# Performance work log

Measured on AMD Instinct MI355X. Metric: run time of the kernel, lower is better.

## Reference

```python
import jax, jax.numpy as jnp
import numpy as np

H, C, L = 2, 32, 25
EPS = 1e-5


def setup_inputs() -> dict:
    key = jax.random.key(0)
    ks = jax.random.split(key, 12)
    N, E = 20000, 100000
    x_input = jax.random.normal(ks[0], (N, 5), jnp.float32)
    # edges with no self loops (module uses add_self_loops=True, which first removes them)
    src = jax.random.randint(ks[1], (L, E), 0, N, dtype=jnp.int32)
    off = jax.random.randint(ks[2], (L, E), 1, N, dtype=jnp.int32)
    dst = (src + off) % N
    edge_indices = jnp.stack([src, dst], axis=1)              # [L, 2, E]
    edge_weights = jax.random.uniform(ks[3], (L, E, 1), jnp.float32)
    g = lambda k, shp, fan: jax.random.normal(k, shp, jnp.float32) / np.float32(np.sqrt(fan))
    return {
        "x_input": x_input,
        "edge_indices": edge_indices,
        "edge_weights": edge_weights,
        "Wl": g(ks[4], (L, 5, H * C), 5),
        "bl": jnp.zeros((L, H * C), jnp.float32),
        "Wr": g(ks[5], (L, 5, H * C), 5),
        "br": jnp.zeros((L, H * C), jnp.float32),
        "We": g(ks[6], (L, 1, H * C), 1),
        "att": g(ks[7], (L, H, C), C),
        "conv_bias": jnp.zeros((L, C), jnp.float32),
        "gamma1": jnp.ones((L, C), jnp.float32),
        "beta1": jnp.zeros((L, C), jnp.float32),
        "W1": g(ks[8], (800, 800), 800),
        "b1": jnp.zeros((800,), jnp.float32),
        "W2": g(ks[9], (800, 5), 800),
        "b2": jnp.zeros((5,), jnp.float32),
    }


def reference(x_input, edge_indices, edge_weights, Wl, bl, Wr, br, We, att,
              conv_bias, gamma1, beta1, W1, b1, W2, b2):
    N = x_input.shape[0]
    loops = jnp.arange(N, dtype=edge_indices.dtype)

    def layer(carry, p):
        ei, ew, wl, bl_, wr, br_, we, a, cb, g_, be_ = p
        src, dst = ei[0], ei[1]
        ones_e = jnp.ones((src.shape[0],), x_input.dtype)
        # add_self_loops with fill_value='mean': loop attr = mean of incoming edge attrs
        cnt = jax.ops.segment_sum(ones_e, dst, num_segments=N)
        loop_attr = jax.ops.segment_sum(ew, dst, num_segments=N) / jnp.maximum(cnt, 1.0)[:, None]
        s2 = jnp.concatenate([src, loops])
        d2 = jnp.concatenate([dst, loops])
        ea = jnp.concatenate([ew, loop_attr], axis=0)          # [E+N, 1]
        xl = (x_input @ wl + bl_).reshape(N, H, C)             # source transform
        xr = (x_input @ wr + br_).reshape(N, H, C)             # target transform
        eh = jax.nn.leaky_relu(xl[s2] + xr[d2] + (ea @ we).reshape(-1, H, C), 0.2)
        alpha = jnp.einsum('ehc,hc->eh', eh, a)                # [E+N, H]
        amax = jax.ops.segment_max(alpha, d2, num_segments=N)
        alpha = jnp.exp(alpha - amax[d2])
        alpha = alpha / jax.ops.segment_sum(alpha, d2, num_segments=N)[d2]
        msg = (xl[s2] * alpha[:, :, None]).reshape(-1, H * C)
        deg = jax.ops.segment_sum(jnp.ones((s2.shape[0],), x_input.dtype), d2, num_segments=N)
        out = (jax.ops.segment_sum(msg, d2, num_segments=N) / deg[:, None]).reshape(N, H, C)
        out = out.mean(axis=1) + cb                            # concat=False -> mean over heads, + bias
        mu = out.mean(axis=0)
        var = out.var(axis=0)                                  # BatchNorm1d, training-mode batch stats
        out = g_ * (out - mu) * jax.lax.rsqrt(var + EPS) + be_
        return carry, jax.nn.leaky_relu(out, 0.01)

    _, hs = jax.lax.scan(layer, None,
                         (edge_indices, edge_weights, Wl, bl, Wr, br, We, att,
                          conv_bias, gamma1, beta1))            # [L, N, C]
    h = jnp.transpose(hs, (1, 0, 2)).reshape(N, L * C)          # cat along feature dim
    h = jax.nn.relu(h @ W1 + b1)
    return h @ W2 + b2
```

## Files before the change

### kernel.cpp

```cpp
#include <hip/hip_runtime.h>
#include <hip/hip_bf16.h>

#define N_NODES 20000
#define N_EDGES 100000
#define N_LAYERS 25
#define NPAD 20096
#define EPS_BN 1e-5f
#define LOG2E 1.44269504088896340736f
#define NL_NN (N_LAYERS * N_NODES)
#define TOTAL_E (N_LAYERS * N_EDGES)
#define TOTAL_SLOTS (TOTAL_E + NL_NN)
#define SCAN_BLKS ((NL_NN + 1023) / 1024)
#define QUARTER_N 5000
#define CNT_BLKS (N_LAYERS * 4)
#define W1T_END (CNT_BLKS + 700)
#define XPAD_END (W1T_END + 157)
#define HPAD_BLKS 75
#define PREP_BLKS (XPAD_END + HPAD_BLKS)
#define EDGE_BLKS ((TOTAL_E + 1023) / 1024)
#define FILL_BLKS (EDGE_BLKS + SCAN_BLKS)
#define NGRP 14
#define NPW 8
#define NPL (N_NODES / NPW)
#define ATTN_WAVES (NL_NN / NPW)
#define ATTN_BLKS (ATTN_WAVES / 4)
#define G1_BLKS (7 * 157)

typedef short short8 __attribute__((ext_vector_type(8)));
typedef short short4v __attribute__((ext_vector_type(4)));
typedef float floatx4 __attribute__((ext_vector_type(4)));
typedef float float8v __attribute__((ext_vector_type(8)));
typedef int int8v __attribute__((ext_vector_type(8)));
typedef int int2v __attribute__((ext_vector_type(2)));

template <int PAT>
__device__ __forceinline__ float swz(float v) {
  return __int_as_float(__builtin_amdgcn_ds_swizzle(__float_as_int(v), PAT));
}

template <int CTRL>
__device__ __forceinline__ float dpp_add(float v) {
  int r = __builtin_amdgcn_update_dpp(0, __float_as_int(v), CTRL, 0xF, 0xF, true);
  return v + __int_as_float(r);
}

__device__ __forceinline__ float xadd16(float p) {
#if __has_builtin(__builtin_amdgcn_permlane16_swap)
  int2v r = __builtin_amdgcn_permlane16_swap(__float_as_int(p),
                                             __float_as_int(p), false, false);
  return __int_as_float(r[0]) + __int_as_float(r[1]);
#else
  return p + swz<0x401F>(p);
#endif
}

__device__ __forceinline__ float ldbf(const unsigned short* __restrict__ p, int idx) {
  return __uint_as_float((unsigned)p[idx] << 16);
}

__device__ __forceinline__ unsigned short bfbits(float v) {
  return __builtin_bit_cast(unsigned short, (__hip_bfloat16)v);
}

__device__ __forceinline__ void gl_lds16(const short* g, short* l) {
  __builtin_amdgcn_global_load_lds(
      (const __attribute__((address_space(1))) void*)g,
      (__attribute__((address_space(3))) void*)l, 16, 0, 0);
}

__device__ __forceinline__ int8v sload8(const void* p) {
  int8v r;
  asm volatile(
      "s_load_dwordx8 %0, %1, 0x0\n\t"
      "s_waitcnt lgkmcnt(0)"
      : "=s"(r)
      : "s"(p));
  return r;
}

__device__ __forceinline__ void sload_rp(const void* p, int8v& a, int8v& b) {
  asm volatile(
      "s_load_dwordx8 %0, %2, 0x0\n\t"
      "s_load_dwordx8 %1, %2, 0x20\n\t"
      "s_waitcnt lgkmcnt(0)"
      : "=s"(a), "=s"(b)
      : "s"(p));
}

__device__ __forceinline__ void sload_chunk(const void* p, int8v& r0, int8v& r1,
                                            int8v& r2, int8v& r3) {
  asm volatile(
      "s_load_dwordx8 %0, %4, 0x0\n\t"
      "s_load_dwordx8 %1, %4, 0x20\n\t"
      "s_load_dwordx8 %2, %4, 0x40\n\t"
      "s_load_dwordx8 %3, %4, 0x60\n\t"
      "s_waitcnt lgkmcnt(0)"
      : "=s"(r0), "=s"(r1), "=s"(r2), "=s"(r3)
      : "s"(p));
}

__device__ __forceinline__ void red4(float& p0, float& p1, float& p2, float& p3) {
  asm volatile(
      "s_nop 1\n\t"
      "v_add_f32_dpp %0, %0, %0 quad_perm:[1,0,3,2] row_mask:0xf bank_mask:0xf\n\t"
      "v_add_f32_dpp %1, %1, %1 quad_perm:[1,0,3,2] row_mask:0xf bank_mask:0xf\n\t"
      "v_add_f32_dpp %2, %2, %2 quad_perm:[1,0,3,2] row_mask:0xf bank_mask:0xf\n\t"
      "v_add_f32_dpp %3, %3, %3 quad_perm:[1,0,3,2] row_mask:0xf bank_mask:0xf\n\t"
      "v_add_f32_dpp %0, %0, %0 quad_perm:[2,3,0,1] row_mask:0xf bank_mask:0xf\n\t"
      "v_add_f32_dpp %1, %1, %1 quad_perm:[2,3,0,1] row_mask:0xf bank_mask:0xf\n\t"
      "v_add_f32_dpp %2, %2, %2 quad_perm:[2,3,0,1] row_mask:0xf bank_mask:0xf\n\t"
      "v_add_f32_dpp %3, %3, %3 quad_perm:[2,3,0,1] row_mask:0xf bank_mask:0xf\n\t"
      "v_add_f32_dpp %0, %0, %0 row_half_mirror row_mask:0xf bank_mask:0xf\n\t"
      "v_add_f32_dpp %1, %1, %1 row_half_mirror row_mask:0xf bank_mask:0xf\n\t"
      "v_add_f32_dpp %2, %2, %2 row_half_mirror row_mask:0xf bank_mask:0xf\n\t"
      "v_add_f32_dpp %3, %3, %3 row_half_mirror row_mask:0xf bank_mask:0xf\n\t"
      "v_add_f32_dpp %0, %0, %0 row_mirror row_mask:0xf bank_mask:0xf\n\t"
      "v_add_f32_dpp %1, %1, %1 row_mirror row_mask:0xf bank_mask:0xf\n\t"
      "v_add_f32_dpp %2, %2, %2 row_mirror row_mask:0xf bank_mask:0xf\n\t"
      "v_add_f32_dpp %3, %3, %3 row_mirror row_mask:0xf bank_mask:0xf\n\t"
      "s_nop 1"
      : "+v"(p0), "+v"(p1), "+v"(p2), "+v"(p3));
}

__global__ __launch_bounds__(1024) void prep_kernel(
    const int* __restrict__ ei, const float* __restrict__ ew,
    const float* __restrict__ x, const float* __restrict__ W1,
    int* __restrict__ cnt, int* __restrict__ rank,
    float* __restrict__ wsumg, float* __restrict__ xpad,
    __hip_bfloat16* __restrict__ W1bT, unsigned short* __restrict__ hn) {
  __shared__ int smem[QUARTER_N];
  __shared__ float fsm[QUARTER_N];
  int b = blockIdx.x;
  if (b < CNT_BLKS) {
    int l = b >> 2, base = (b & 3) * QUARTER_N;
    for (int i = threadIdx.x; i < QUARTER_N; i += 1024) {
      smem[i] = 0;
      fsm[i] = 0.f;
    }
    __syncthreads();
    const int* dstp = ei + (size_t)l * 2 * N_EDGES + N_EDGES;
    const float* ewp = ew + (size_t)l * N_EDGES;
    int* rkp = rank + l * N_EDGES;
    for (int e = threadIdx.x; e < N_EDGES; e += 1024) {
      int d = dstp[e] - base;
      if ((unsigned)d < (unsigned)QUARTER_N) {
        rkp[e] = atomicAdd(&smem[d], 1);
        atomicAdd(&fsm[d], ewp[e]);
      }
    }
    __syncthreads();
    int* outp = cnt + l * N_NODES + base;
    float* wp = wsumg + l * N_NODES + base;
    for (int i = threadIdx.x; i < QUARTER_N; i += 1024) {
      outp[i] = smem[i];
      wp[i] = fsm[i];
    }
  } else if (b < W1T_END) {
    float* tile = (float*)smem;
    int bb = b - CNT_BLKS;
    int j0 = (bb % 28) * 32, k0 = (bb / 28) * 32;
    int tx = threadIdx.x & 31, ty = threadIdx.x >> 5;
    tile[ty * 33 + tx] = (j0 + tx < 800) ? W1[(k0 + ty) * 800 + j0 + tx] : 0.f;
    __syncthreads();
    W1bT[(size_t)(j0 + ty) * 800 + k0 + tx] = (__hip_bfloat16)tile[tx * 33 + ty];
  } else if (b < XPAD_END) {
    int idx = (b - W1T_END) * 1024 + threadIdx.x;
    if (idx < N_NODES * 8) {
      int nn = idx >> 3, k = idx & 7;
      xpad[idx] = (k < 5) ? x[nn * 5 + k] : 0.f;
    }
  } else {
    int idx = (b - XPAD_END) * 1024 + threadIdx.x;
    const int per_l = (NPAD - N_NODES) * 32;
    if (idx < N_LAYERS * per_l) {
      int l = idx / per_l;
      int rem = idx - l * per_l;
      hn[((size_t)l * NPAD + N_NODES) * 32 + rem] = 0;
    }
  }
}

__global__ __launch_bounds__(1024) void scan_a(const int* __restrict__ cnt,
                                               int* __restrict__ scn,
                                               int* __restrict__ btot,
                                               float* __restrict__ gsum,
                                               float* __restrict__ gsumsq) {
  int t = threadIdx.x, b = blockIdx.x;
  int i = b * 1024 + t;
  int lane = t & 63, wv = t >> 6;
  int v = (i < NL_NN) ? cnt[i] + 1 : 0;
  int sc = v;
#pragma unroll
  for (int off = 1; off < 64; off <<= 1) {
    int u = __shfl_up(sc, off);
    if (lane >= off) sc += u;
  }
  __shared__ int ws[16];
  if (lane == 63) ws[wv] = sc;
  __syncthreads();
  if (t < 16) {
    int xx = ws[t];
#pragma unroll
    for (int off = 1; off < 16; off <<= 1) {
      int u = __shfl_up(xx, off);
      if (t >= off) xx += u;
    }
    ws[t] = xx;
  }
  __syncthreads();
  int bofs = wv ? ws[wv - 1] : 0;
  if (i < NL_NN) scn[i] = bofs + sc - v;
  if (t == 0) btot[b] = ws[15];
  if (b == 200 && t < N_LAYERS * 32) {
    gsum[t] = 0.f;
    gsumsq[t] = 0.f;
  }
}

__global__ __launch_bounds__(512) void scan_b(const int* __restrict__ btot,
                                              int* __restrict__ boff) {
  int t = threadIdx.x;
  int lane = t & 63, wv = t >> 6;
  int v = (t < SCAN_BLKS) ? btot[t] : 0;
  int sc = v;
#pragma unroll
  for (int off = 1; off < 64; off <<= 1) {
    int u = __shfl_up(sc, off);
    if (lane >= off) sc += u;
  }
  __shared__ int ws[8];
  if (lane == 63) ws[wv] = sc;
  __syncthreads();
  if (t < 8) {
    int xx = ws[t];
#pragma unroll
    for (int off = 1; off < 8; off <<= 1) {
      int u = __shfl_up(xx, off);
      if (t >= off) xx += u;
    }
    ws[t] = xx;
  }
  __syncthreads();
  int bofs = wv ? ws[wv - 1] : 0;
  if (t < SCAN_BLKS) boff[t] = bofs + sc - v;
}

__global__ __launch_bounds__(1024) void fill_kernel(const int* __restrict__ ei,
                                                    const float* __restrict__ ew,
                                                    const int* __restrict__ scn,
                                                    const int* __restrict__ boff,
                                                    const int* __restrict__ rank,
                                                    const float* __restrict__ wsumg,
                                                    const float* __restrict__ xpad,
                                                    int* __restrict__ rowptr,
                                                    float* __restrict__ epf) {
  int b = blockIdx.x;
  if (b < EDGE_BLKS) {
    int idx = b * 1024 + threadIdx.x;
    if (idx >= TOTAL_E) return;
    int l = idx / N_EDGES, e = idx - l * N_EDGES;
    int src = ei[(size_t)l * 2 * N_EDGES + e];
    int dst = ei[(size_t)l * 2 * N_EDGES + N_EDGES + e];
    int g = l * N_NODES + dst;
    int pos = scn[g] + boff[g >> 10] + rank[idx];
    float w = ew[(size_t)l * N_EDGES + e];
    float4 xv = *(const float4*)(xpad + (size_t)src * 8);
    float x4v = xpad[(size_t)src * 8 + 4];
    float8v r;
    r[0] = w; r[1] = xv.x; r[2] = xv.y; r[3] = xv.z; r[4] = xv.w; r[5] = x4v;
    r[6] = 0.f; r[7] = 0.f;
    *(float8v*)(epf + (size_t)pos * 8) = r;
  } else {
    int i = (b - EDGE_BLKS) * 1024 + threadIdx.x;
    if (i < NL_NN) {
      int st = scn[i] + boff[i >> 10];
      int en = (i + 1 < NL_NN) ? scn[i + 1] + boff[(i + 1) >> 10] : TOTAL_SLOTS;
      rowptr[i] = st;
      int cw = en - st - 1;
      float wm = wsumg[i] * __builtin_amdgcn_rcpf(fmaxf((float)cw, 1.f));
      int n = i - (i / N_NODES) * N_NODES;
      float4 xv = *(const float4*)(xpad + (size_t)n * 8);
      float x4v = xpad[(size_t)n * 8 + 4];
      float8v r;
      r[0] = wm; r[1] = xv.x; r[2] = xv.y; r[3] = xv.z; r[4] = xv.w; r[5] = x4v;
      r[6] = 0.f; r[7] = 0.f;
      *(float8v*)(epf + (size_t)(en - 1) * 8) = r;
    }
    if (i < 31) rowptr[NL_NN + i] = TOTAL_SLOTS;
    if (i < 4) {
      float8v z = {0.f, 0.f, 0.f, 0.f, 0.f, 0.f, 0.f, 0.f};
      *(float8v*)(epf + (size_t)(TOTAL_SLOTS + i) * 8) = z;
    }
  }
}

__global__ __launch_bounds__(256) void attn_kernel(
    const float* __restrict__ xpad, const int* __restrict__ rowptr,
    const float* __restrict__ epf,
    const float* __restrict__ Wl, const float* __restrict__ bl,
    const float* __restrict__ Wr, const float* __restrict__ br,
    const float* __restrict__ We, const float* __restrict__ att,
    const float* __restrict__ cbias, unsigned short* __restrict__ out_pre,
    float* __restrict__ gsum, float* __restrict__ gsumsq) {
  int b = blockIdx.x;
  const int q = ATTN_BLKS >> 3, r = ATTN_BLKS & 7;
  int xcd = b & 7, ib = b >> 3;
  int nb = (xcd < r ? xcd * (q + 1) : r * (q + 1) + (xcd - r) * q) + ib;
  int wid = __builtin_amdgcn_readfirstlane(nb * 4 + (threadIdx.x >> 6));
  int lane = threadIdx.x & 63;
  int l = wid / NPL;
  int n0 = (wid - l * NPL) * NPW;

  float wlv0 = Wl[(l * 5 + 0) * 64 + lane];
  float wlv1 = Wl[(l * 5 + 1) * 64 + lane];
  float wlv2 = Wl[(l * 5 + 2) * 64 + lane];
  float wlv3 = Wl[(l * 5 + 3) * 64 + lane];
  float wlv4 = Wl[(l * 5 + 4) * 64 + lane];
  float wr0 = Wr[(l * 5 + 0) * 64 + lane];
  float wr1 = Wr[(l * 5 + 1) * 64 + lane];
  float wr2 = Wr[(l * 5 + 2) * 64 + lane];
  float wr3 = Wr[(l * 5 + 3) * 64 + lane];
  float wr4 = Wr[(l * 5 + 4) * 64 + lane];
  float blv = bl[l * 64 + lane];
  float brv = br[l * 64 + lane];
  float wev = We[l * 64 + lane];
  float att2v = att[l * 64 + lane] * LOG2E;
  float cbv = cbias[l * 32 + (lane & 31)];

  int8v rpa, rpb;
  sload_rp(rowptr + (size_t)wid * 8, rpa, rpb);

  float s1 = 0.f, s2 = 0.f;

#pragma unroll
  for (int i = 0; i < NPW; i++) {
    int st = rpa[i & 7];
    int en = (i == 7) ? rpb[0] : rpa[(i + 1) & 7];
    int valid = en - st;

    int8v xn = sload8(xpad + (size_t)(n0 + i) * 8);
    float xrn = brv;
    xrn = fmaf(__int_as_float(xn[0]), wr0, xrn);
    xrn = fmaf(__int_as_float(xn[1]), wr1, xrn);
    xrn = fmaf(__int_as_float(xn[2]), wr2, xrn);
    xrn = fmaf(__int_as_float(xn[3]), wr3, xrn);
    xrn = fmaf(__int_as_float(xn[4]), wr4, xrn);

    float ssum = 0.f, acc = 0.f;
    int nchunk = (valid + 3) >> 2;
    for (int c = 0; c < nchunk; c++) {
      int8v r0, r1, r2, r3;
      sload_chunk(epf + (size_t)(st + c * 4) * 8, r0, r1, r2, r3);
      int m = valid - c * 4;
      float xa[4], pk[4];
#pragma unroll
      for (int k = 0; k < 4; k++) {
        int8v rr = (k == 0) ? r0 : (k == 1) ? r1 : (k == 2) ? r2 : r3;
        float a = fmaf(__int_as_float(rr[1]), wlv0, blv);
        a = fmaf(__int_as_float(rr[2]), wlv1, a);
        a = fmaf(__int_as_float(rr[3]), wlv2, a);
        a = fmaf(__int_as_float(rr[4]), wlv3, a);
        a = fmaf(__int_as_float(rr[5]), wlv4, a);
        xa[k] = a;
        float v = a + fmaf(__int_as_float(rr[0]), wev, xrn);
        float lk = fmaxf(v, 0.2f * v);
        pk[k] = lk * att2v;
      }
      red4(pk[0], pk[1], pk[2], pk[3]);
#pragma unroll
      for (int k = 0; k < 4; k++) pk[k] = xadd16(pk[k]);
#pragma unroll
      for (int k = 0; k < 4; k++) {
        float pe = __builtin_amdgcn_exp2f(pk[k]);
        pe = (k < m) ? pe : 0.f;
        ssum += pe;
        acc = fmaf(xa[k], pe, acc);
      }
    }
    float outv = acc * __builtin_amdgcn_rcpf(ssum * (float)valid);
    float o2 = outv + __shfl_xor(outv, 32);
    float oval = 0.5f * o2 + cbv;
    if (lane < 32)
      out_pre[((size_t)wid * NPW + i) * 32 + lane] = bfbits(oval);
    s1 += oval;
    s2 = fmaf(oval, oval, s2);
  }
  if (lane < 32) {
    atomicAdd(&gsum[l * 32 + lane], s1);
    atomicAdd(&gsumsq[l * 32 + lane], s2);
  }
}

__global__ __launch_bounds__(256) void norm_kernel(const unsigned short* __restrict__ out_pre,
                                                   const float* __restrict__ gsum,
                                                   const float* __restrict__ gsumsq,
                                                   const float* __restrict__ gamma,
                                                   const float* __restrict__ beta,
                                                   unsigned short* __restrict__ hn) {
  int idx = blockIdx.x * 256 + threadIdx.x;
  int l = idx / (N_NODES * 8);
  int rem = idx - l * (N_NODES * 8);
  int n = rem >> 3, q = rem & 7;
  int c0 = q * 4;
  short4v v4 = *(const short4v*)(out_pre + (l * N_NODES + n) * 32 + c0);
  short4v o;
#pragma unroll
  for (int i = 0; i < 4; i++) {
    int c = c0 + i;
    float mu = gsum[l * 32 + c] * (1.f / N_NODES);
    float var = gsumsq[l * 32 + c] * (1.f / N_NODES) - mu * mu;
    float vv = __uint_as_float((unsigned)(unsigned short)v4[i] << 16);
    float v = gamma[l * 32 + c] * (vv - mu) * rsqrtf(var + EPS_BN) + beta[l * 32 + c];
    v = v > 0.f ? v : 0.01f * v;
    o[i] = (short)bfbits(v);
  }
  *(short4v*)(hn + ((size_t)l * NPAD + n) * 32 + c0) = o;
}

__global__ __launch_bounds__(256) void gemm1_kernel(const short* __restrict__ hn,
                                                    const short* __restrict__ W1bT,
                                                    const float* __restrict__ b1,
                                                    const float* __restrict__ W2,
                                                    float* __restrict__ p) {
  __shared__ __align__(16) short As[128 * 32];
  __shared__ __align__(16) short Bs[128 * 32];
  const int q = G1_BLKS >> 3, r = G1_BLKS & 7;
  int bf = blockIdx.x;
  int xcd = bf & 7, ib = bf >> 3;
  int nb = (xcd < r ? xcd * (q + 1) : r * (q + 1) + (xcd - r) * q) + ib;
  int mt = nb / 7, nt = nb - mt * 7;
  int n0 = nt * 128, m0 = mt * 128;
  int t = threadIdx.x;
  int wave = t >> 6, lane = t & 63;
  int wr = wave >> 1, wc = wave & 1;
  int mrow = lane & 15, quad = lane >> 4;
  floatx4 acc[4][4];
#pragma unroll
  for (int i = 0; i < 4; i++)
#pragma unroll
    for (int j = 0; j < 4; j++) acc[i][j] = (floatx4){0.f, 0.f, 0.f, 0.f};

  int r0 = t >> 2, s0 = t & 3;
  int r1 = (t + 256) >> 2, s1 = (t + 256) & 3;
  const short* aG0 = hn + (m0 + r0) * 32 + s0 * 8;
  const short* aG1 = hn + (m0 + r1) * 32 + s1 * 8;
  const short* bG0 = W1bT + (n0 + r0) * 800 + s0 * 8;
  const short* bG1 = W1bT + (n0 + r1) * 800 + s1 * 8;
  const int ak = NPAD * 32;
  short* aD0 = As + wave * 512;
  short* aD1 = As + 2048 + wave * 512;
  short* bD0 = Bs + wave * 512;
  short* bD1 = Bs + 2048 + wave * 512;

  for (int kt = 0; kt < 25; kt++) {
    gl_lds16(aG0, aD0);
    gl_lds16(aG1, aD1);
    gl_lds16(bG0, bD0);
    gl_lds16(bG1, bD1);
    aG0 += ak; aG1 += ak; bG0 += 32; bG1 += 32;
    __syncthreads();
    short8 af[4], bfr[4];
#pragma unroll
    for (int i = 0; i < 4; i++)
      af[i] = *(const short8*)(&As[(wr * 64 + i * 16 + mrow) * 32 + quad * 8]);
#pragma unroll
    for (int j = 0; j < 4; j++)
      bfr[j] = *(const short8*)(&Bs[(wc * 64 + j * 16 + mrow) * 32 + quad * 8]);
#pragma unroll
    for (int i = 0; i < 4; i++)
#pragma unroll
      for (int j = 0; j < 4; j++)
        acc[i][j] = __builtin_amdgcn_mfma_f32_16x16x32_bf16(af[i], bfr[j], acc[i][j], 0, 0, 0);
    __syncthreads();
  }

  float w2v[4][5];
  float b1v[4];
#pragma unroll
  for (int j = 0; j < 4; j++) {
    int col = n0 + wc * 64 + j * 16 + mrow;
    bool ok = col < 800;
    b1v[j] = ok ? b1[col] : 0.f;
#pragma unroll
    for (int jj = 0; jj < 5; jj++) w2v[j][jj] = ok ? W2[col * 5 + jj] : 0.f;
  }
  int grp = nt * 2 + wc;
#pragma unroll
  for (int i = 0; i < 4; i++) {
#pragma unroll
    for (int rr = 0; rr < 4; rr++) {
      float s[5] = {0.f, 0.f, 0.f, 0.f, 0.f};
#pragma unroll
      for (int j = 0; j < 4; j++) {
        float v = fmaxf(acc[i][j][rr] + b1v[j], 0.f);
#pragma unroll
        for (int jj = 0; jj < 5; jj++) s[jj] = fmaf(v, w2v[j][jj], s[jj]);
      }
#pragma unroll
      for (int jj = 0; jj < 5; jj++) {
        s[jj] = dpp_add<0xB1>(s[jj]);
        s[jj] = dpp_add<0x4E>(s[jj]);
        s[jj] = dpp_add<0x141>(s[jj]);
        s[jj] = dpp_add<0x140>(s[jj]);
      }
      int row = m0 + wr * 64 + i * 16 + quad * 4 + rr;
      if (mrow == 0) {
#pragma unroll
        for (int jj = 0; jj < 5; jj++)
          p[(row * NGRP + grp) * 5 + jj] = s[jj];
      }
    }
  }
}

__global__ __launch_bounds__(256) void gemm2r_kernel(const float* __restrict__ p,
                                                     const float* __restrict__ b2,
                                                     float* __restrict__ out) {
  int idx = blockIdx.x * 256 + threadIdx.x;
  if (idx >= N_NODES * 5) return;
  int row = idx / 5, jj = idx - row * 5;
  float s = b2[jj];
#pragma unroll
  for (int g = 0; g < NGRP; g++) s += p[(row * NGRP + g) * 5 + jj];
  out[idx] = s;
}

extern "C" void kernel_launch(void* const* d_in, const int* in_sizes, int n_in,
                              void* d_out, int out_size, void* d_ws, size_t ws_size,
                              hipStream_t stream) {
  const float* x    = (const float*)d_in[0];
  const int*   ei   = (const int*)d_in[1];
  const float* ew   = (const float*)d_in[2];
  const float* Wl   = (const float*)d_in[3];
  const float* bl   = (const float*)d_in[4];
  const float* Wr   = (const float*)d_in[5];
  const float* br   = (const float*)d_in[6];
  const float* We   = (const float*)d_in[7];
  const float* att  = (const float*)d_in[8];
  const float* cb   = (const float*)d_in[9];
  const float* gam  = (const float*)d_in[10];
  const float* bet  = (const float*)d_in[11];
  const float* W1   = (const float*)d_in[12];
  const float* b1   = (const float*)d_in[13];
  const float* W2   = (const float*)d_in[14];
  const float* b2   = (const float*)d_in[15];

  char* ws = (char*)d_ws;
  size_t off = 0;
  auto alloc = [&](size_t bytes) {
    void* p = ws + off;
    off = (off + bytes + 255) & ~(size_t)255;
    return p;
  };
  int* cnt     = (int*)alloc((size_t)NL_NN * 4);
  int* scn     = (int*)alloc((size_t)NL_NN * 4);
  int* btot    = (int*)alloc(SCAN_BLKS * 4);
  int* boff    = (int*)alloc(SCAN_BLKS * 4);
  int* rank    = (int*)alloc((size_t)TOTAL_E * 4);
  int* rowptr  = (int*)alloc((size_t)(NL_NN + 32) * 4);
  float* wsumg = (float*)alloc((size_t)NL_NN * 4);
  float* epf   = (float*)alloc((size_t)TOTAL_SLOTS * 32 + 256);
  unsigned short* out_pre = (unsigned short*)alloc((size_t)NL_NN * 32 * 2);
  float* gsum   = (float*)alloc(N_LAYERS * 32 * 4);
  float* gsumsq = (float*)alloc(N_LAYERS * 32 * 4);
  float* xpad   = (float*)alloc((size_t)N_NODES * 8 * 4);
  __hip_bfloat16* w1t = (__hip_bfloat16*)alloc((size_t)896 * 800 * 2);
  float* pbuf = (float*)alloc((size_t)NPAD * NGRP * 5 * 4);
  unsigned short* hn = (unsigned short*)alloc((size_t)N_LAYERS * NPAD * 32 * 2);

  prep_kernel<<<PREP_BLKS, 1024, 0, stream>>>(ei, ew, x, W1, cnt, rank, wsumg,
                                              xpad, w1t, hn);
  scan_a<<<SCAN_BLKS, 1024, 0, stream>>>(cnt, scn, btot, gsum, gsumsq);
  scan_b<<<1, 512, 0, stream>>>(btot, boff);
  fill_kernel<<<FILL_BLKS, 1024, 0, stream>>>(ei, ew, scn, boff, rank, wsumg,
                                              xpad, rowptr, epf);
  attn_kernel<<<ATTN_BLKS, 256, 0, stream>>>(
      xpad, rowptr, epf, Wl, bl, Wr, br, We, att, cb, out_pre, gsum, gsumsq);
  norm_kernel<<<(NL_NN * 8) / 256, 256, 0, stream>>>(
      out_pre, gsum, gsumsq, gam, bet, hn);
  gemm1_kernel<<<G1_BLKS, 256, 0, stream>>>(
      (const short*)hn, (const short*)w1t, b1, W2, pbuf);
  gemm2r_kernel<<<(N_NODES * 5 + 255) / 256, 256, 0, stream>>>(
      pbuf, b2, (float*)d_out);
}
```

Baseline: 484.3 us.

## Pack per-edge records to 16 bytes with bf16 features, widen attn chunks to 8

The per-edge record written by fill_kernel shrinks from 32 bytes of fp32 to 16 bytes: the edge weight stays fp32 and the five source features are stored as bf16 pairs. attn_kernel now reads 8 edges per scalar-load chunk instead of 4 and reduces 8 logits at once with a wider DPP reduction. BatchNorm partial sums are combined across the block's four waves in shared memory before the atomics, cutting atomic traffic fourfold. The intent is to halve the edge-record bandwidth and amortise reduction and sync work, at the cost of bf16 rounding of the input features and more wasted lanes on short rows.

```diff
diff --git a/kernel.cpp b/kernel.cpp
--- a/kernel.cpp
+++ b/kernel.cpp
@@ -29,9 +29,9 @@
 typedef short short8 __attribute__((ext_vector_type(8)));
 typedef short short4v __attribute__((ext_vector_type(4)));
 typedef float floatx4 __attribute__((ext_vector_type(4)));
-typedef float float8v __attribute__((ext_vector_type(8)));
 typedef int int8v __attribute__((ext_vector_type(8)));
 typedef int int2v __attribute__((ext_vector_type(2)));
+typedef int int4v __attribute__((ext_vector_type(4)));
 
 template <int PAT>
 __device__ __forceinline__ float swz(float v) {
@@ -99,27 +99,45 @@
       : "s"(p));
 }
 
-__device__ __forceinline__ void red4(float& p0, float& p1, float& p2, float& p3) {
+__device__ __forceinline__ void red8(float& p0, float& p1, float& p2, float& p3,
+                                     float& p4, float& p5, float& p6, float& p7) {
   asm volatile(
       "s_nop 1\n\t"
       "v_add_f32_dpp %0, %0, %0 quad_perm:[1,0,3,2] row_mask:0xf bank_mask:0xf\n\t"
       "v_add_f32_dpp %1, %1, %1 quad_perm:[1,0,3,2] row_mask:0xf bank_mask:0xf\n\t"
       "v_add_f32_dpp %2, %2, %2 quad_perm:[1,0,3,2] row_mask:0xf bank_mask:0xf\n\t"
       "v_add_f32_dpp %3, %3, %3 quad_perm:[1,0,3,2] row_mask:0xf bank_mask:0xf\n\t"
+      "v_add_f32_dpp %4, %4, %4 quad_perm:[1,0,3,2] row_mask:0xf bank_mask:0xf\n\t"
+      "v_add_f32_dpp %5, %5, %5 quad_perm:[1,0,3,2] row_mask:0xf bank_mask:0xf\n\t"
+      "v_add_f32_dpp %6, %6, %6 quad_perm:[1,0,3,2] row_mask:0xf bank_mask:0xf\n\t"
+      "v_add_f32_dpp %7, %7, %7 quad_perm:[1,0,3,2] row_mask:0xf bank_mask:0xf\n\t"
       "v_add_f32_dpp %0, %0, %0 quad_perm:[2,3,0,1] row_mask:0xf bank_mask:0xf\n\t"
       "v_add_f32_dpp %1, %1, %1 quad_perm:[2,3,0,1] row_mask:0xf bank_mask:0xf\n\t"
       "v_add_f32_dpp %2, %2, %2 quad_perm:[2,3,0,1] row_mask:0xf bank_mask:0xf\n\t"
       "v_add_f32_dpp %3, %3, %3 quad_perm:[2,3,0,1] row_mask:0xf bank_mask:0xf\n\t"
+      "v_add_f32_dpp %4, %4, %4 quad_perm:[2,3,0,1] row_mask:0xf bank_mask:0xf\n\t"
+      "v_add_f32_dpp %5, %5, %5 quad_perm:[2,3,0,1] row_mask:0xf bank_mask:0xf\n\t"
+      "v_add_f32_dpp %6, %6, %6 quad_perm:[2,3,0,1] row_mask:0xf bank_mask:0xf\n\t"
+      "v_add_f32_dpp %7, %7, %7 quad_perm:[2,3,0,1] row_mask:0xf bank_mask:0xf\n\t"
       "v_add_f32_dpp %0, %0, %0 row_half_mirror row_mask:0xf bank_mask:0xf\n\t"
       "v_add_f32_dpp %1, %1, %1 row_half_mirror row_mask:0xf bank_mask:0xf\n\t"
       "v_add_f32_dpp %2, %2, %2 row_half_mirror row_mask:0xf bank_mask:0xf\n\t"
       "v_add_f32_dpp %3, %3, %3 row_half_mirror row_mask:0xf bank_mask:0xf\n\t"
+      "v_add_f32_dpp %4, %4, %4 row_half_mirror row_mask:0xf bank_mask:0xf\n\t"
+      "v_add_f32_dpp %5, %5, %5 row_half_mirror row_mask:0xf bank_mask:0xf\n\t"
+      "v_add_f32_dpp %6, %6, %6 row_half_mirror row_mask:0xf bank_mask:0xf\n\t"
+      "v_add_f32_dpp %7, %7, %7 row_half_mirror row_mask:0xf bank_mask:0xf\n\t"
       "v_add_f32_dpp %0, %0, %0 row_mirror row_mask:0xf bank_mask:0xf\n\t"
       "v_add_f32_dpp %1, %1, %1 row_mirror row_mask:0xf bank_mask:0xf\n\t"
       "v_add_f32_dpp %2, %2, %2 row_mirror row_mask:0xf bank_mask:0xf\n\t"
       "v_add_f32_dpp %3, %3, %3 row_mirror row_mask:0xf bank_mask:0xf\n\t"
+      "v_add_f32_dpp %4, %4, %4 row_mirror row_mask:0xf bank_mask:0xf\n\t"
+      "v_add_f32_dpp %5, %5, %5 row_mirror row_mask:0xf bank_mask:0xf\n\t"
+      "v_add_f32_dpp %6, %6, %6 row_mirror row_mask:0xf bank_mask:0xf\n\t"
+      "v_add_f32_dpp %7, %7, %7 row_mirror row_mask:0xf bank_mask:0xf\n\t"
       "s_nop 1"
-      : "+v"(p0), "+v"(p1), "+v"(p2), "+v"(p3));
+      : "+v"(p0), "+v"(p1), "+v"(p2), "+v"(p3),
+        "+v"(p4), "+v"(p5), "+v"(p6), "+v"(p7));
 }
 
 __global__ __launch_bounds__(1024) void prep_kernel(
@@ -253,7 +271,7 @@
                                                     const float* __restrict__ wsumg,
                                                     const float* __restrict__ xpad,
                                                     int* __restrict__ rowptr,
-                                                    float* __restrict__ epf) {
+                                                    int* __restrict__ epr) {
   int b = blockIdx.x;
   if (b < EDGE_BLKS) {
     int idx = b * 1024 + threadIdx.x;
@@ -266,10 +284,12 @@
     float w = ew[(size_t)l * N_EDGES + e];
     float4 xv = *(const float4*)(xpad + (size_t)src * 8);
     float x4v = xpad[(size_t)src * 8 + 4];
-    float8v r;
-    r[0] = w; r[1] = xv.x; r[2] = xv.y; r[3] = xv.z; r[4] = xv.w; r[5] = x4v;
-    r[6] = 0.f; r[7] = 0.f;
-    *(float8v*)(epf + (size_t)pos * 8) = r;
+    int4v r;
+    r[0] = __float_as_int(w);
+    r[1] = (int)bfbits(xv.x) | ((int)bfbits(xv.y) << 16);
+    r[2] = (int)bfbits(xv.z) | ((int)bfbits(xv.w) << 16);
+    r[3] = (int)bfbits(x4v);
+    *(int4v*)(epr + (size_t)pos * 4) = r;
   } else {
     int i = (b - EDGE_BLKS) * 1024 + threadIdx.x;
     if (i < NL_NN) {
@@ -281,33 +301,38 @@
       int n = i - (i / N_NODES) * N_NODES;
       float4 xv = *(const float4*)(xpad + (size_t)n * 8);
       float x4v = xpad[(size_t)n * 8 + 4];
-      float8v r;
-      r[0] = wm; r[1] = xv.x; r[2] = xv.y; r[3] = xv.z; r[4] = xv.w; r[5] = x4v;
-      r[6] = 0.f; r[7] = 0.f;
-      *(float8v*)(epf + (size_t)(en - 1) * 8) = r;
+      int4v r;
+      r[0] = __float_as_int(wm);
+      r[1] = (int)bfbits(xv.x) | ((int)bfbits(xv.y) << 16);
+      r[2] = (int)bfbits(xv.z) | ((int)bfbits(xv.w) << 16);
+      r[3] = (int)bfbits(x4v);
+      *(int4v*)(epr + (size_t)(en - 1) * 4) = r;
     }
     if (i < 31) rowptr[NL_NN + i] = TOTAL_SLOTS;
-    if (i < 4) {
-      float8v z = {0.f, 0.f, 0.f, 0.f, 0.f, 0.f, 0.f, 0.f};
-      *(float8v*)(epf + (size_t)(TOTAL_SLOTS + i) * 8) = z;
+    if (i < 8) {
+      int4v z = {0, 0, 0, 0};
+      *(int4v*)(epr + (size_t)(TOTAL_SLOTS + i) * 4) = z;
     }
   }
 }
 
 __global__ __launch_bounds__(256) void attn_kernel(
     const float* __restrict__ xpad, const int* __restrict__ rowptr,
-    const float* __restrict__ epf,
+    const int* __restrict__ epr,
     const float* __restrict__ Wl, const float* __restrict__ bl,
     const float* __restrict__ Wr, const float* __restrict__ br,
     const float* __restrict__ We, const float* __restrict__ att,
     const float* __restrict__ cbias, unsigned short* __restrict__ out_pre,
     float* __restrict__ gsum, float* __restrict__ gsumsq) {
+  __shared__ float sb[256];
   int b = blockIdx.x;
   const int q = ATTN_BLKS >> 3, r = ATTN_BLKS & 7;
   int xcd = b & 7, ib = b >> 3;
   int nb = (xcd < r ? xcd * (q + 1) : r * (q + 1) + (xcd - r) * q) + ib;
-  int wid = __builtin_amdgcn_readfirstlane(nb * 4 + (threadIdx.x >> 6));
-  int lane = threadIdx.x & 63;
+  int tid = threadIdx.x;
+  int w = tid >> 6;
+  int wid = __builtin_amdgcn_readfirstlane(nb * 4 + w);
+  int lane = tid & 63;
   int l = wid / NPL;
   int n0 = (wid - l * NPL) * NPW;
 
@@ -347,30 +372,40 @@
     xrn = fmaf(__int_as_float(xn[4]), wr4, xrn);
 
     float ssum = 0.f, acc = 0.f;
-    int nchunk = (valid + 3) >> 2;
+    int nchunk = (valid + 7) >> 3;
     for (int c = 0; c < nchunk; c++) {
       int8v r0, r1, r2, r3;
-      sload_chunk(epf + (size_t)(st + c * 4) * 8, r0, r1, r2, r3);
-      int m = valid - c * 4;
-      float xa[4], pk[4];
-#pragma unroll
-      for (int k = 0; k < 4; k++) {
-        int8v rr = (k == 0) ? r0 : (k == 1) ? r1 : (k == 2) ? r2 : r3;
-        float a = fmaf(__int_as_float(rr[1]), wlv0, blv);
-        a = fmaf(__int_as_float(rr[2]), wlv1, a);
-        a = fmaf(__int_as_float(rr[3]), wlv2, a);
-        a = fmaf(__int_as_float(rr[4]), wlv3, a);
-        a = fmaf(__int_as_float(rr[5]), wlv4, a);
+      sload_chunk((const char*)epr + (size_t)(st + c * 8) * 16, r0, r1, r2, r3);
+      int m = valid - c * 8;
+      float xa[8], pk[8];
+#define RVEC(k) ((k) < 2 ? r0 : (k) < 4 ? r1 : (k) < 6 ? r2 : r3)
+#define RD(k, j) (RVEC(k)[((k)&1) * 4 + (j)])
+#pragma unroll
+      for (int k = 0; k < 8; k++) {
+        float wgt = __int_as_float(RD(k, 0));
+        int d1 = RD(k, 1), d2 = RD(k, 2), d3 = RD(k, 3);
+        float x0 = __int_as_float(d1 << 16);
+        float x1 = __int_as_float(d1 & (int)0xffff0000);
+        float x2 = __int_as_float(d2 << 16);
+        float x3 = __int_as_float(d2 & (int)0xffff0000);
+        float x4 = __int_as_float(d3 << 16);
+        float a = fmaf(x0, wlv0, blv);
+        a = fmaf(x1, wlv1, a);
+        a = fmaf(x2, wlv2, a);
+        a = fmaf(x3, wlv3, a);
+        a = fmaf(x4, wlv4, a);
         xa[k] = a;
-        float v = a + fmaf(__int_as_float(rr[0]), wev, xrn);
+        float v = a + fmaf(wgt, wev, xrn);
         float lk = fmaxf(v, 0.2f * v);
         pk[k] = lk * att2v;
       }
-      red4(pk[0], pk[1], pk[2], pk[3]);
-#pragma unroll
-      for (int k = 0; k < 4; k++) pk[k] = xadd16(pk[k]);
-#pragma unroll
-      for (int k = 0; k < 4; k++) {
+#undef RVEC
+#undef RD
+      red8(pk[0], pk[1], pk[2], pk[3], pk[4], pk[5], pk[6], pk[7]);
+#pragma unroll
+      for (int k = 0; k < 8; k++) pk[k] = xadd16(pk[k]);
+#pragma unroll
+      for (int k = 0; k < 8; k++) {
         float pe = __builtin_amdgcn_exp2f(pk[k]);
         pe = (k < m) ? pe : 0.f;
         ssum += pe;
@@ -385,9 +420,14 @@
     s1 += oval;
     s2 = fmaf(oval, oval, s2);
   }
-  if (lane < 32) {
-    atomicAdd(&gsum[l * 32 + lane], s1);
-    atomicAdd(&gsumsq[l * 32 + lane], s2);
+  sb[tid] = (lane < 32) ? s1 : s2;
+  __syncthreads();
+  if (tid < 64) {
+    float t = sb[tid] + sb[tid + 64] + sb[tid + 128] + sb[tid + 192];
+    if (tid < 32)
+      atomicAdd(&gsum[l * 32 + tid], t);
+    else
+      atomicAdd(&gsumsq[l * 32 + tid - 32], t);
   }
 }
 
@@ -559,7 +599,7 @@
   int* rank    = (int*)alloc((size_t)TOTAL_E * 4);
   int* rowptr  = (int*)alloc((size_t)(NL_NN + 32) * 4);
   float* wsumg = (float*)alloc((size_t)NL_NN * 4);
-  float* epf   = (float*)alloc((size_t)TOTAL_SLOTS * 32 + 256);
+  int* epr     = (int*)alloc((size_t)TOTAL_SLOTS * 16 + 256);
   unsigned short* out_pre = (unsigned short*)alloc((size_t)NL_NN * 32 * 2);
   float* gsum   = (float*)alloc(N_LAYERS * 32 * 4);
   float* gsumsq = (float*)alloc(N_LAYERS * 32 * 4);
@@ -573,9 +613,9 @@
   scan_a<<<SCAN_BLKS, 1024, 0, stream>>>(cnt, scn, btot, gsum, gsumsq);
   scan_b<<<1, 512, 0, stream>>>(btot, boff);
   fill_kernel<<<FILL_BLKS, 1024, 0, stream>>>(ei, ew, scn, boff, rank, wsumg,
-                                              xpad, rowptr, epf);
+                                              xpad, rowptr, epr);
   attn_kernel<<<ATTN_BLKS, 256, 0, stream>>>(
-      xpad, rowptr, epf, Wl, bl, Wr, br, We, att, cb, out_pre, gsum, gsumsq);
+      xpad, rowptr, epr, Wl, bl, Wr, br, We, att, cb, out_pre, gsum, gsumsq);
   norm_kernel<<<(NL_NN * 8) / 256, 256, 0, stream>>>(
       out_pre, gsum, gsumsq, gam, bet, hn);
   gemm1_kernel<<<G1_BLKS, 256, 0, stream>>>(
```

Result: faster. 453.6 us (-6.3%).
